# Performance work log

Hardware: AMD Instinct MI355X
Metric: run time of the kernel (lower is better)

The kernel has to match this reference:

```python
import jax, jax.numpy as jnp
import numpy as np

TEMPERATURE = 0.5
SCALE_BY_TEMPERATURE = True
CURV = 0.05

N = 8192
D = 128
N_PRIMARY = 32
N_SECONDARY = 16


def setup_inputs() -> dict:
    key = jax.random.key(0)
    k1, k2, k3 = jax.random.split(key, 3)
    features = jax.random.normal(k1, (N, D), dtype=jnp.float32)
    primary_labels = jax.random.randint(k2, (N,), 0, N_PRIMARY)
    secondary_labels = jax.random.randint(k3, (N,), 0, N_SECONDARY)
    return {"features": features, "primary_labels": primary_labels,
            "secondary_labels": secondary_labels}


def _hyp_contrastive_loss(features, primary_labels, secondary_labels):
    c = CURV
    sqrt_c = c ** 0.5
    n = features.shape[0]

    # L2 normalize (torch F.normalize with eps=1e-12)
    nrm = jnp.maximum(jnp.linalg.norm(features, axis=1, keepdims=True), 1e-12)
    f = features / nrm

    # Pairwise mobius_add(-f[j], f[i]) at [i, j]. With x = -f[j], y = f[i]:
    #   num = (1 + 2c<x,y> + c|y|^2) x + (1 - c|x|^2) y,   den = 1 + 2c<x,y> + c^2|x|^2|y|^2
    # We only need ||num||/den, so expand ||num||^2 algebraically to avoid an
    # [N, N, D] intermediate (same math, exact).
    n2 = jnp.sum(f * f, axis=1)            # [N], ~1 after normalize
    s = f @ f.T                            # [N, N] <f_i, f_j>
    xy = -s                                # <x, y>
    x2 = n2[None, :]                       # |x|^2 = |f_j|^2
    y2 = n2[:, None]                       # |y|^2 = |f_i|^2

    A = 1.0 + 2.0 * c * xy + c * y2
    B = 1.0 - c * x2
    den = jnp.maximum(1.0 + 2.0 * c * xy + c * c * x2 * y2, 1e-15)
    num_sq = jnp.maximum(A * A * x2 + 2.0 * A * B * xy + B * B * y2, 0.0)
    norm_diff = sqrt_c * jnp.sqrt(num_sq) / den           # [N, N]

    # artanh with clamp (pm.artanh clamps argument below 1)
    distance = jnp.arctanh(jnp.clip(norm_diff, 0.0, 1.0 - 1e-7)) * 2.0 / sqrt_c

    anchor_dot_contrast = -distance / TEMPERATURE
    logits_max = jax.lax.stop_gradient(
        jnp.max(anchor_dot_contrast, axis=1, keepdims=True))
    logits = anchor_dot_contrast - logits_max
    exp_logits = jnp.exp(logits)

    pmask = (primary_labels[:, None] == primary_labels[None, :]).astype(f.dtype)
    smask = (secondary_labels[:, None] == secondary_labels[None, :]).astype(f.dtype)
    combined = jnp.minimum(pmask + smask, 1.0)

    eye = jnp.eye(n, dtype=f.dtype)
    positives_mask = combined * (1.0 - eye)
    negatives_mask = 1.0 - combined

    num_pos = jnp.sum(positives_mask, axis=1)             # [N]
    valid = num_pos > 0

    pos_contrib = jnp.sum(exp_logits * positives_mask, axis=1)
    neg_contrib = jnp.sum(exp_logits * negatives_mask, axis=1)
    denominator = pos_contrib + neg_contrib + 1e-8        # [N]

    log_probs = logits - jnp.log(denominator)[:, None]
    row_sum = jnp.sum(log_probs * positives_mask, axis=1)
    per_row = jnp.where(valid, row_sum / jnp.maximum(num_pos, 1.0), 0.0)

    n_valid = jnp.sum(valid.astype(f.dtype))
    loss = -jnp.sum(per_row) / jnp.maximum(n_valid, 1.0)  # mean over valid rows
    loss = jnp.where(n_valid > 0, loss, 0.0)
    if SCALE_BY_TEMPERATURE:
        loss = loss * TEMPERATURE
    return jnp.nan_to_num(loss, nan=0.0, posinf=0.0, neginf=0.0)


def reference(features, primary_labels, secondary_labels):
    return _hyp_contrastive_loss(features, primary_labels, secondary_labels)
```

## Files before the change

### kernel.cpp

```cpp
#include <hip/hip_runtime.h>
#include <hip/hip_bf16.h>

#define NN 8192
#define DD 128

typedef short short8 __attribute__((ext_vector_type(8)));
typedef __bf16 bf16x8 __attribute__((ext_vector_type(8)));
typedef float f32x4 __attribute__((ext_vector_type(4)));
typedef float f32x2 __attribute__((ext_vector_type(2)));

#define MKc (-0.110803324099723f)
#define PKc (0.110803324099723f)
#define C1Kc (1.110803324099723f)
#define KEc (-8.944271909999159f)
#define KLc (-6.199696797323639f)

__global__ __launch_bounds__(256) void prep_kernel(const float* __restrict__ x,
                                                   __hip_bfloat16* __restrict__ fb,
                                                   float* __restrict__ totg,
                                                   float* __restrict__ tposg) {
  int r = threadIdx.x >> 4, sub = threadIdx.x & 15;
  int row = blockIdx.x * 16 + r;
  const float4 a = *(const float4*)(x + (size_t)row * DD + sub * 8);
  const float4 b = *(const float4*)(x + (size_t)row * DD + sub * 8 + 4);
  float ss = a.x * a.x + a.y * a.y + a.z * a.z + a.w * a.w +
             b.x * b.x + b.y * b.y + b.z * b.z + b.w * b.w;
  for (int off = 1; off < 16; off <<= 1) ss += __shfl_xor(ss, off, 16);
  float inv = 1.0f / fmaxf(sqrtf(ss), 1e-12f);
  float va[8] = {a.x, a.y, a.z, a.w, b.x, b.y, b.z, b.w};
  short8 h;
  for (int j = 0; j < 8; j++) {
    __hip_bfloat16 t = __float2bfloat16(va[j] * inv);
    h[j] = __builtin_bit_cast(short, t);
  }
  *(short8*)((short*)fb + (size_t)row * DD + sub * 8) = h;
  if (threadIdx.x < 16) {
    totg[blockIdx.x * 16 + threadIdx.x] = 0.f;
    tposg[blockIdx.x * 16 + threadIdx.x] = 0.f;
  }
}

__global__ __launch_bounds__(256, 2) void fused_kernel(
    const __hip_bfloat16* __restrict__ fbg,
    const int* __restrict__ plab, const int* __restrict__ slab,
    float* __restrict__ totg, float* __restrict__ tposg) {
  __shared__ int plc[512], slc[512];

  const int tid = threadIdx.x;
  const int w = tid >> 6;
  const int lane = tid & 63;
  const int lrow = lane & 15;
  const int quad = lane >> 4;
  const int R0 = blockIdx.y * 128;
  const int C0 = blockIdx.x * 512;
  const bool hasDiag = (blockIdx.y >> 2) == blockIdx.x;

  for (int i = tid; i < 512; i += 256) {
    plc[i] = plab[C0 + i];
    slc[i] = slab[C0 + i];
  }

  bf16x8 af[2][4];
  int plr[2][4], slr[2][4];
  for (int strip = 0; strip < 2; strip++) {
    const short* fa = (const short*)fbg + (size_t)(R0 + w * 32 + strip * 16 + lrow) * DD;
    for (int kk = 0; kk < 4; kk++)
      af[strip][kk] = __builtin_bit_cast(bf16x8, *(const short8*)(fa + kk * 32 + quad * 8));
    for (int r = 0; r < 4; r++) {
      int rowg = R0 + w * 32 + strip * 16 + quad * 4 + r;
      plr[strip][r] = plab[rowg];
      slr[strip][r] = slab[rowg];
    }
  }
  __syncthreads();

  const f32x2 MK2 = {MKc, MKc}, PK2 = {PKc, PKc}, C1K2 = {C1Kc, C1Kc};
  const f32x2 KE2 = {KEc, KEc}, ZERO2 = {0.f, 0.f}, EPS2 = {1e-30f, 1e-30f};
  const f32x2 ONE2 = {1.f, 1.f};

  f32x2 t2[2][2], g2[2][2];
  for (int s_ = 0; s_ < 2; s_++)
    for (int p = 0; p < 2; p++) { t2[s_][p] = ZERO2; g2[s_][p] = ZERO2; }

  const short* bp = (const short*)fbg + (size_t)(C0 + lrow) * DD + quad * 8;
  int colg = C0 + lrow;

  for (int ct = 0; ct < 32; ct++) {
    bf16x8 bf[4];
    for (int kk = 0; kk < 4; kk++)
      bf[kk] = __builtin_bit_cast(bf16x8, *(const short8*)(bp + kk * 32));
    bp += 16 * DD;

    f32x4 acc[2];
    for (int strip = 0; strip < 2; strip++) {
      f32x4 a0 = {0.f, 0.f, 0.f, 0.f};
      for (int kk = 0; kk < 4; kk++)
        a0 = __builtin_amdgcn_mfma_f32_16x16x32_bf16(af[strip][kk], bf[kk], a0, 0, 0, 0);
      acc[strip] = a0;
    }

    const int lc = ct * 16 + lrow;
    const int pc = plc[lc];
    const int sc = slc[lc];

    for (int strip = 0; strip < 2; strip++) {
      for (int p = 0; p < 2; p++) {
        f32x2 s2 = {acc[strip][2 * p], acc[strip][2 * p + 1]};
        f32x2 tK = __builtin_elementwise_fma(s2, MK2, PK2);
        tK = __builtin_elementwise_max(tK, ZERO2);
        f32x2 dk = __builtin_elementwise_fma(s2, MK2, C1K2);
        f32x2 m = __builtin_elementwise_max(tK * dk, EPS2);
        f32x2 rq = {__builtin_amdgcn_rsqf(m.x), __builtin_amdgcn_rsqf(m.y)};
        f32x2 nd = tK * rq;
        f32x2 p1 = nd + ONE2;
        f32x2 rr = p1 * p1 * dk;
        f32x2 lg = {__log2f(rr.x), __log2f(rr.y)};
        f32x2 el = KE2 * lg;
        f32x2 e = {exp2f(el.x), exp2f(el.y)};
        const int r0 = 2 * p, r1 = 2 * p + 1;
        bool same0 = (pc == plr[strip][r0]) || (sc == slr[strip][r0]);
        bool same1 = (pc == plr[strip][r1]) || (sc == slr[strip][r1]);
        if (hasDiag) {
          int rg0 = R0 + w * 32 + strip * 16 + quad * 4 + r0;
          bool off0 = (colg != rg0);
          bool off1 = (colg != rg0 + 1);
          f32x2 em = {off0 ? e.x : 0.f, off1 ? e.y : 0.f};
          f32x2 lm = {(same0 && off0) ? lg.x : 0.f, (same1 && off1) ? lg.y : 0.f};
          t2[strip][p] += em;
          g2[strip][p] += lm;
        } else {
          f32x2 lm = {same0 ? lg.x : 0.f, same1 ? lg.y : 0.f};
          t2[strip][p] += e;
          g2[strip][p] += lm;
        }
      }
    }
    colg += 16;
  }

  for (int strip = 0; strip < 2; strip++) {
    for (int r = 0; r < 4; r++) {
      float t = t2[strip][r >> 1][r & 1];
      float g = g2[strip][r >> 1][r & 1];
      for (int off = 1; off < 16; off <<= 1) {
        t += __shfl_xor(t, off, 16);
        g += __shfl_xor(g, off, 16);
      }
      if (lrow == 0) {
        int rowg = R0 + w * 32 + strip * 16 + quad * 4 + r;
        atomicAdd(&totg[rowg], t);
        atomicAdd(&tposg[rowg], g);
      }
    }
  }
}

__global__ __launch_bounds__(1024) void finalize_k(const float* __restrict__ totg,
                                                   const float* __restrict__ tposg,
                                                   const int* __restrict__ plab,
                                                   const int* __restrict__ slab,
                                                   float* __restrict__ out) {
  __shared__ int hist[512];
  __shared__ int cntP[32], cntS[16];
  __shared__ float redP[16], redV[16];
  const int tid = threadIdx.x;
  if (tid < 512) hist[tid] = 0;
  __syncthreads();
  for (int i = tid; i < NN; i += 1024)
    atomicAdd(&hist[plab[i] * 16 + slab[i]], 1);
  __syncthreads();
  if (tid < 32) {
    int s = 0;
    for (int j = 0; j < 16; j++) s += hist[tid * 16 + j];
    cntP[tid] = s;
  } else if (tid >= 64 && tid < 80) {
    int s = 0;
    for (int j = 0; j < 32; j++) s += hist[j * 16 + (tid - 64)];
    cntS[tid - 64] = s;
  }
  __syncthreads();
  float accP = 0.f, accV = 0.f;
  for (int i = tid; i < NN; i += 1024) {
    int pl = plab[i], sl = slab[i];
    int np = cntP[pl] + cntS[sl] - hist[pl * 16 + sl] - 1;
    if (np > 0) {
      accP += (KLc * tposg[i]) / (float)np - __logf(totg[i] + 1e-8f);
      accV += 1.f;
    }
  }
  for (int off = 32; off; off >>= 1) {
    accP += __shfl_xor(accP, off, 64);
    accV += __shfl_xor(accV, off, 64);
  }
  int wv = tid >> 6;
  if ((tid & 63) == 0) { redP[wv] = accP; redV[wv] = accV; }
  __syncthreads();
  if (tid == 0) {
    float sp = 0.f, sv = 0.f;
    for (int j = 0; j < 16; j++) { sp += redP[j]; sv += redV[j]; }
    float loss = -(sp / fmaxf(sv, 1.0f)) * 0.5f;
    if (sv <= 0.0f || !__builtin_isfinite(loss)) loss = 0.0f;
    out[0] = loss;
  }
}

extern "C" void kernel_launch(void* const* d_in, const int* in_sizes, int n_in,
                              void* d_out, int out_size, void* d_ws, size_t ws_size,
                              hipStream_t stream) {
  const float* x = (const float*)d_in[0];
  const int* pl = (const int*)d_in[1];
  const int* sl = (const int*)d_in[2];
  char* ws = (char*)d_ws;
  __hip_bfloat16* fb = (__hip_bfloat16*)ws;
  float* totg = (float*)(ws + 2097152);
  float* tposg = (float*)(ws + 2129920);

  prep_kernel<<<NN / 16, 256, 0, stream>>>(x, fb, totg, tposg);
  fused_kernel<<<dim3(16, 64), 256, 0, stream>>>(fb, pl, sl, totg, tposg);
  finalize_k<<<1, 1024, 0, stream>>>(totg, tposg, pl, sl, (float*)d_out);
}
```

Baseline: 136.7 us.

## Exploit symmetry of pairwise distance matrix to compute only lower-triangle tiles

The pairwise distance depends only on the symmetric dot product, so the kernel now launches only tiles on or below the diagonal (544 instead of 1024) and feeds each computed exp and masked log term into both row and column sums. Column partial sums are reduced across quads with shuffles, collected in shared memory per wave, and then atomically added to the global column accumulators. Diagonal tiles mask to strictly lower entries. This roughly halves the MFMA and transcendental work, at the cost of extra shared-memory traffic, shuffles, more atomics, and a serial loop to decode the tile index.

```diff
diff --git a/kernel.cpp b/kernel.cpp
--- a/kernel.cpp
+++ b/kernel.cpp
@@ -45,19 +45,29 @@
     const int* __restrict__ plab, const int* __restrict__ slab,
     float* __restrict__ totg, float* __restrict__ tposg) {
   __shared__ int plc[512], slc[512];
+  __shared__ float colT_l[4 * 512];
+  __shared__ float colG_l[4 * 512];
 
   const int tid = threadIdx.x;
   const int w = tid >> 6;
   const int lane = tid & 63;
   const int lrow = lane & 15;
   const int quad = lane >> 4;
-  const int R0 = blockIdx.y * 128;
-  const int C0 = blockIdx.x * 512;
-  const bool hasDiag = (blockIdx.y >> 2) == blockIdx.x;
+
+  int J = 0, rem = blockIdx.x;
+  while (rem >= 64 - 4 * J) { rem -= 64 - 4 * J; J++; }
+  const int I = 4 * J + rem;
+  const bool needMask = (I < 4 * J + 4);
+  const int R0 = I * 128;
+  const int C0 = J * 512;
 
   for (int i = tid; i < 512; i += 256) {
     plc[i] = plab[C0 + i];
     slc[i] = slab[C0 + i];
+  }
+  for (int i = lane; i < 512; i += 64) {
+    colT_l[w * 512 + i] = 0.f;
+    colG_l[w * 512 + i] = 0.f;
   }
 
   bf16x8 af[2][4];
@@ -102,6 +112,8 @@
     const int lc = ct * 16 + lrow;
     const int pc = plc[lc];
     const int sc = slc[lc];
+
+    f32x2 colE = ZERO2, colL = ZERO2;
 
     for (int strip = 0; strip < 2; strip++) {
       for (int p = 0; p < 2; p++) {
@@ -120,20 +132,36 @@
         const int r0 = 2 * p, r1 = 2 * p + 1;
         bool same0 = (pc == plr[strip][r0]) || (sc == slr[strip][r0]);
         bool same1 = (pc == plr[strip][r1]) || (sc == slr[strip][r1]);
-        if (hasDiag) {
+        f32x2 em, lm;
+        if (needMask) {
           int rg0 = R0 + w * 32 + strip * 16 + quad * 4 + r0;
-          bool off0 = (colg != rg0);
-          bool off1 = (colg != rg0 + 1);
-          f32x2 em = {off0 ? e.x : 0.f, off1 ? e.y : 0.f};
-          f32x2 lm = {(same0 && off0) ? lg.x : 0.f, (same1 && off1) ? lg.y : 0.f};
-          t2[strip][p] += em;
-          g2[strip][p] += lm;
+          bool ok0 = (colg < rg0);
+          bool ok1 = (colg < rg0 + 1);
+          em.x = ok0 ? e.x : 0.f;
+          em.y = ok1 ? e.y : 0.f;
+          lm.x = (same0 && ok0) ? lg.x : 0.f;
+          lm.y = (same1 && ok1) ? lg.y : 0.f;
         } else {
-          f32x2 lm = {same0 ? lg.x : 0.f, same1 ? lg.y : 0.f};
-          t2[strip][p] += e;
-          g2[strip][p] += lm;
+          em = e;
+          lm.x = same0 ? lg.x : 0.f;
+          lm.y = same1 ? lg.y : 0.f;
         }
+        t2[strip][p] += em;
+        g2[strip][p] += lm;
+        colE += em;
+        colL += lm;
       }
+    }
+
+    float cE = colE.x + colE.y;
+    float cL = colL.x + colL.y;
+    cE += __shfl_xor(cE, 16, 64);
+    cE += __shfl_xor(cE, 32, 64);
+    cL += __shfl_xor(cL, 16, 64);
+    cL += __shfl_xor(cL, 32, 64);
+    if (quad == 0) {
+      colT_l[w * 512 + lc] += cE;
+      colG_l[w * 512 + lc] += cL;
     }
     colg += 16;
   }
@@ -153,6 +181,14 @@
       }
     }
   }
+
+  __syncthreads();
+  for (int i = tid; i < 512; i += 256) {
+    float sE = colT_l[i] + colT_l[512 + i] + colT_l[1024 + i] + colT_l[1536 + i];
+    float sL = colG_l[i] + colG_l[512 + i] + colG_l[1024 + i] + colG_l[1536 + i];
+    atomicAdd(&totg[C0 + i], sE);
+    atomicAdd(&tposg[C0 + i], sL);
+  }
 }
 
 __global__ __launch_bounds__(1024) void finalize_k(const float* __restrict__ totg,
@@ -216,6 +252,6 @@
   float* tposg = (float*)(ws + 2129920);
 
   prep_kernel<<<NN / 16, 256, 0, stream>>>(x, fb, totg, tposg);
-  fused_kernel<<<dim3(16, 64), 256, 0, stream>>>(fb, pl, sl, totg, tposg);
+  fused_kernel<<<544, 256, 0, stream>>>(fb, pl, sl, totg, tposg);
   finalize_k<<<1, 1024, 0, stream>>>(totg, tposg, pl, sl, (float*)d_out);
 }
```

Result: faster. 123.8 us (-9.4%).
